# Kernel optimization log

Hardware: AMD Instinct MI355X
Metric: run time of the kernel (lower is better)

Reference implementation:

```python
import jax, jax.numpy as jnp
import numpy as np

B, CIN, NF, COUT, H, W = 128, 64, 16, 256, 20, 20


def _warp(features, f):
    # features: (B, Cin, r, c), f: (r, c, 2) flow offsets
    r, c = features.shape[2], features.shape[3]
    grid = jnp.stack(
        jnp.meshgrid(jnp.arange(r, dtype=f.dtype), jnp.arange(c, dtype=f.dtype), indexing='ij'),
        axis=-1,
    )  # (r, c, 2) base index map
    idx = grid + f  # index_map += inverse, inverse == flow[i] after double negation
    base = jnp.floor(idx)
    frac = jax.lax.stop_gradient(idx - base)  # torch detaches s and t
    s, t = frac[..., 0], frac[..., 1]
    b = base.astype(jnp.int32)
    bx, by = b[..., 0], b[..., 1]
    padded = jnp.pad(features, ((0, 0), (0, 0), (1, 1), (1, 1)))  # zero pad by 1

    def gather(ix, iy):
        cx = jnp.clip(ix, 0, r)
        cy = jnp.clip(iy, 0, c)
        return padded[:, :, cx + 1, cy + 1]  # (B, Cin, r, c)

    # NOTE: weight for base_10 is s*(1-t) in the original source (apparent bug,
    # should be (1-s)*t) -- replicated here for faithfulness.
    w00 = (1 - s) * (1 - t)
    w01 = s * (1 - t)
    w10 = s * (1 - t)
    w11 = s * t
    return (gather(bx, by) * w00 + gather(bx + 1, by) * w01
            + gather(bx, by + 1) * w10 + gather(bx + 1, by + 1) * w11)


def setup_inputs() -> dict:
    key = jax.random.key(0)
    k1, k2, k3, k4 = jax.random.split(key, 4)
    x = jax.random.normal(k1, (B, CIN, H, W), dtype=jnp.float32)
    flow = jax.random.normal(k2, (NF, H, W, 2), dtype=jnp.float32)
    combinator = jax.random.normal(k3, (COUT, CIN * NF), dtype=jnp.float32) / np.sqrt(CIN * NF)
    bias = jax.random.normal(k4, (COUT,), dtype=jnp.float32) / np.sqrt(CIN * NF)
    return {"x": x, "flow": flow, "combinator": combinator, "bias": bias}


def reference(x, flow, combinator, bias):
    # per-flow bilinear warp, vectorized over the flow axis
    warped = jax.vmap(lambda f: _warp(x, f))(flow)  # (nf, B, Cin, h, w)
    nf, b, cin, h, w = warped.shape
    # permute(1,3,4,2,0).reshape -> columns ordered channel-major, flow-minor
    feat = warped.transpose(1, 3, 4, 2, 0).reshape(b, h, w, cin * nf)
    out = jnp.einsum('bhwk,ok->bhwo', feat, combinator) + bias
    return out.transpose(0, 3, 1, 2)  # (B, Cout, h, w)
```

## Files before the change

### kernel.cpp

```cpp
#include <hip/hip_runtime.h>
#include <hip/hip_fp16.h>
#include <stdint.h>

#define BATCH 128
#define CIN   64
#define NFLOW 16
#define COUT  256
#define HH    20
#define WW    20
#define NPIX  400
#define KTOT  1024
#define PT    100
#define NPT   4
#define NTH   256
#define NFR   7
#define FLR   112

typedef __attribute__((ext_vector_type(8))) short sh8;
typedef __attribute__((ext_vector_type(4))) float f4;

__global__ void prep_w(const float* __restrict__ wg, __half* __restrict__ Wf) {
    int gid = blockIdx.x * 256 + threadIdx.x;
    int j8  = gid & 127;
    int row = gid >> 7;
    int kc16 = j8 >> 2;
    int h    = j8 & 3;
    __half* dst = Wf + ((size_t)(kc16 * 16 + (row >> 4)) * 64 + h * 16 + (row & 15)) * 8;
    #pragma unroll
    for (int j = 0; j < 8; ++j) {
        int kp = j8 * 8 + j;
        int kc = kp >> 6;
        int l  = kp & 63;
        int f  = (kc >> 3) * 8 + (l >> 3);
        int c  = (kc & 7) * 8 + (l & 7);
        dst[j] = __float2half(wg[(size_t)row * KTOT + c * NFLOW + f]);
    }
}

__global__ __launch_bounds__(NTH, 2) void flow_main(
    const float* __restrict__ xg, const __half* __restrict__ Wf,
    const float* __restrict__ flowg, const float* __restrict__ biasg,
    float* __restrict__ outg)
{
    __shared__ __align__(16) __half xb[CIN * NPIX];
    __shared__ __align__(16) __half fl[2][FLR * 64];

    const int bid0 = blockIdx.x;
    const int bid  = (bid0 & 7) * 64 + (bid0 >> 3);
    const int b  = bid >> 2;
    const int pt = bid & 3;
    const int p0 = pt * PT;

    const int tid  = threadIdx.x;
    const int wv   = tid >> 6;
    const int lane = tid & 63;
    const int lr   = lane & 15;
    const int hq   = lane >> 4;

    const float* xsrc = xg + (size_t)b * (CIN * NPIX);

    #pragma unroll
    for (int it = 0; it < 13; ++it) {
        int idx = it * NTH + tid;
        if (idx < 3200) {
            int cb  = idx / NPIX;
            int pix = idx - cb * NPIX;
            const float* s = xsrc + (size_t)(cb * 8) * NPIX + pix;
            __half2 h0 = __floats2half2_rn(s[0 * NPIX], s[1 * NPIX]);
            __half2 h1 = __floats2half2_rn(s[2 * NPIX], s[3 * NPIX]);
            __half2 h2 = __floats2half2_rn(s[4 * NPIX], s[5 * NPIX]);
            __half2 h3 = __floats2half2_rn(s[6 * NPIX], s[7 * NPIX]);
            uint4 pk;
            pk.x = __builtin_bit_cast(uint32_t, h0);
            pk.y = __builtin_bit_cast(uint32_t, h1);
            pk.z = __builtin_bit_cast(uint32_t, h2);
            pk.w = __builtin_bit_cast(uint32_t, h3);
            *(uint4*)&xb[(size_t)idx * 8] = pk;
        }
    }

    __half2 w2_[4][4];
    int     pb_[4][4];
    int     fo_[4];

    auto build_tables = [&](int fb) {
        #pragma unroll
        for (int g = 0; g < 4; ++g) {
            int it = g & 1;
            if (it == 0 || lane < PT - 64) {
                int fi = wv * 2 + (g >> 1);
                int p  = it * 64 + lane;
                int f  = fb * 8 + fi;
                int gp = p0 + p;
                int i = gp / WW;
                int j = gp - i * WW;
                float fx = flowg[((f * HH + i) * WW + j) * 2 + 0];
                float fy = flowg[((f * HH + i) * WW + j) * 2 + 1];
                float ax = (float)i + fx;
                float ay = (float)j + fy;
                float bxf = floorf(ax), byf = floorf(ay);
                float s = ax - bxf, t = ay - byf;
                int ibx = (int)bxf, iby = (int)byf;
                float w00 = (1.f - s) * (1.f - t);
                float w01 = s * (1.f - t);
                float w10 = s * (1.f - t);
                float w11 = s * t;
                int cx0 = min(max(ibx, 0), HH);
                int cx1 = min(max(ibx + 1, 0), HH);
                int cy0 = min(max(iby, 0), WW);
                int cy1 = min(max(iby + 1, 0), WW);
                int v0 = (cx0 < HH) & (cy0 < WW);
                int v1 = (cx1 < HH) & (cy0 < WW);
                int v2 = (cx0 < HH) & (cy1 < WW);
                int v3 = (cx1 < HH) & (cy1 < WW);
                w2_[g][0] = __half2half2(__float2half(v0 ? w00 : 0.f));
                w2_[g][1] = __half2half2(__float2half(v1 ? w01 : 0.f));
                w2_[g][2] = __half2half2(__float2half(v2 ? w10 : 0.f));
                w2_[g][3] = __half2half2(__float2half(v3 ? w11 : 0.f));
                pb_[g][0] = (v0 ? (cx0 * WW + cy0) : 0) * 16;
                pb_[g][1] = (v1 ? (cx1 * WW + cy0) : 0) * 16;
                pb_[g][2] = (v2 ? (cx0 * WW + cy1) : 0) * 16;
                pb_[g][3] = (v3 ? (cx1 * WW + cy1) : 0) * 16;
                fo_[g] = p * 128 + (((fi) ^ (p & 7)) << 4);
            }
        }
    };

    auto fill = [&](int k) {
        const char* xcb = (const char*)xb + (k & 7) * 6400;
        char* flb = (char*)fl[k & 1];
        #pragma unroll
        for (int g = 0; g < 4; ++g) {
            int it = g & 1;
            if (it == 0 || lane < PT - 64) {
                __half2 s0 = __builtin_bit_cast(__half2, 0u);
                __half2 s1 = s0, s2 = s0, s3 = s0;
                #pragma unroll
                for (int q = 0; q < 4; ++q) {
                    const uint4 d = *(const uint4*)(xcb + pb_[g][q]);
                    __half2 wq = w2_[g][q];
                    s0 = __hfma2(wq, __builtin_bit_cast(__half2, d.x), s0);
                    s1 = __hfma2(wq, __builtin_bit_cast(__half2, d.y), s1);
                    s2 = __hfma2(wq, __builtin_bit_cast(__half2, d.z), s2);
                    s3 = __hfma2(wq, __builtin_bit_cast(__half2, d.w), s3);
                }
                uint4 pk;
                pk.x = __builtin_bit_cast(uint32_t, s0);
                pk.y = __builtin_bit_cast(uint32_t, s1);
                pk.z = __builtin_bit_cast(uint32_t, s2);
                pk.w = __builtin_bit_cast(uint32_t, s3);
                *(uint4*)(flb + fo_[g]) = pk;
            }
        }
    };

    build_tables(0);
    __syncthreads();
    fill(0);
    __syncthreads();

    f4 acc[4][NFR] = {};

    const int q0 = (hq ^ (lr & 7)) << 4;

    for (int kc = 0; kc < 16; ++kc) {
        if (kc == 7) build_tables(1);

        const sh8* wfp = (const sh8*)Wf + (size_t)(2 * kc * 16 + 4 * wv) * 64 + lane;
        sh8 a0_0 = wfp[0],    a0_1 = wfp[64],   a0_2 = wfp[128],  a0_3 = wfp[192];
        sh8 a1_0 = wfp[1024], a1_1 = wfp[1088], a1_2 = wfp[1152], a1_3 = wfp[1216];

        if (kc <= 14) fill(kc + 1);

        const char* flr_b = (const char*)fl[kc & 1];
        __builtin_amdgcn_s_setprio(1);
        #pragma unroll
        for (int nf = 0; nf < NFR; ++nf) {
            int rowb = (nf * 16 + lr) * 128;
            sh8 b0 = *(const sh8*)(flr_b + (rowb + q0));
            sh8 b1 = *(const sh8*)(flr_b + ((rowb + q0) ^ 64));
            acc[0][nf] = __builtin_amdgcn_mfma_f32_16x16x32_f16(a0_0, b0, acc[0][nf], 0, 0, 0);
            acc[1][nf] = __builtin_amdgcn_mfma_f32_16x16x32_f16(a0_1, b0, acc[1][nf], 0, 0, 0);
            acc[2][nf] = __builtin_amdgcn_mfma_f32_16x16x32_f16(a0_2, b0, acc[2][nf], 0, 0, 0);
            acc[3][nf] = __builtin_amdgcn_mfma_f32_16x16x32_f16(a0_3, b0, acc[3][nf], 0, 0, 0);
            acc[0][nf] = __builtin_amdgcn_mfma_f32_16x16x32_f16(a1_0, b1, acc[0][nf], 0, 0, 0);
            acc[1][nf] = __builtin_amdgcn_mfma_f32_16x16x32_f16(a1_1, b1, acc[1][nf], 0, 0, 0);
            acc[2][nf] = __builtin_amdgcn_mfma_f32_16x16x32_f16(a1_2, b1, acc[2][nf], 0, 0, 0);
            acc[3][nf] = __builtin_amdgcn_mfma_f32_16x16x32_f16(a1_3, b1, acc[3][nf], 0, 0, 0);
        }
        __builtin_amdgcn_s_setprio(0);

        __syncthreads();
    }

    float* ob = outg + (size_t)b * (COUT * NPIX) + p0;
    #pragma unroll
    for (int mi = 0; mi < 4; ++mi) {
        #pragma unroll
        for (int r = 0; r < 4; ++r) {
            int m = wv * 64 + mi * 16 + hq * 4 + r;
            float bs = biasg[m];
            #pragma unroll
            for (int nf = 0; nf < NFR; ++nf) {
                if (nf < 6 || lr < 4)
                    ob[(size_t)m * NPIX + nf * 16 + lr] = acc[mi][nf][r] + bs;
            }
        }
    }
}

extern "C" void kernel_launch(void* const* d_in, const int* in_sizes, int n_in,
                              void* d_out, int out_size, void* d_ws, size_t ws_size,
                              hipStream_t stream) {
    const float* x    = (const float*)d_in[0];
    const float* flow = (const float*)d_in[1];
    const float* comb = (const float*)d_in[2];
    const float* bias = (const float*)d_in[3];
    float* out = (float*)d_out;

    __half* Wf = (__half*)d_ws;

    prep_w<<<dim3(128), dim3(256), 0, stream>>>(comb, Wf);
    flow_main<<<dim3(BATCH * NPT), dim3(NTH), 0, stream>>>(x, Wf, flow, bias, out);
}
```

Measured before the change: 50.74 us.

## Split waves into producer/consumer roles and process two pixel tiles per block

Doubles the block to 512 threads, with four waves building the bilinear-warped tiles in LDS and four waves running the MFMA GEMM on the other buffer. Each block now handles two pixel tiles of one batch, so the x-to-half conversion into shared memory is amortized across twice the work and the grid is halved. The intent is to overlap the gather/fill work with matrix-core work. The cost is fewer blocks for the GPU, a per-chunk barrier between roles, and register pressure under the unchanged launch bounds.

```diff
diff --git a/kernel.cpp b/kernel.cpp
--- a/kernel.cpp
+++ b/kernel.cpp
@@ -11,8 +11,7 @@
 #define NPIX  400
 #define KTOT  1024
 #define PT    100
-#define NPT   4
-#define NTH   256
+#define NTH   512
 #define NFR   7
 #define FLR   112
 
@@ -46,13 +45,14 @@
     __shared__ __align__(16) __half fl[2][FLR * 64];
 
     const int bid0 = blockIdx.x;
-    const int bid  = (bid0 & 7) * 64 + (bid0 >> 3);
-    const int b  = bid >> 2;
-    const int pt = bid & 3;
-    const int p0 = pt * PT;
+    const int bid  = (bid0 & 7) * 32 + (bid0 >> 3);
+    const int b  = bid >> 1;
+    const int tp = bid & 1;
 
     const int tid  = threadIdx.x;
     const int wv   = tid >> 6;
+    const bool prod = wv < 4;
+    const int cwv  = wv & 3;
     const int lane = tid & 63;
     const int lr   = lane & 15;
     const int hq   = lane >> 4;
@@ -60,7 +60,7 @@
     const float* xsrc = xg + (size_t)b * (CIN * NPIX);
 
     #pragma unroll
-    for (int it = 0; it < 13; ++it) {
+    for (int it = 0; it < 7; ++it) {
         int idx = it * NTH + tid;
         if (idx < 3200) {
             int cb  = idx / NPIX;
@@ -83,12 +83,12 @@
     int     pb_[4][4];
     int     fo_[4];
 
-    auto build_tables = [&](int fb) {
+    auto build_tables = [&](int fb, int p0) {
         #pragma unroll
         for (int g = 0; g < 4; ++g) {
             int it = g & 1;
             if (it == 0 || lane < PT - 64) {
-                int fi = wv * 2 + (g >> 1);
+                int fi = cwv * 2 + (g >> 1);
                 int p  = it * 64 + lane;
                 int f  = fb * 8 + fi;
                 int gp = p0 + p;
@@ -121,7 +121,7 @@
                 pb_[g][1] = (v1 ? (cx1 * WW + cy0) : 0) * 16;
                 pb_[g][2] = (v2 ? (cx0 * WW + cy1) : 0) * 16;
                 pb_[g][3] = (v3 ? (cx1 * WW + cy1) : 0) * 16;
-                fo_[g] = p * 128 + (((fi) ^ (p & 7)) << 4);
+                fo_[g] = p * 128 + ((fi ^ (p & 7)) << 4);
             }
         }
     };
@@ -154,56 +154,71 @@
         }
     };
 
-    build_tables(0);
     __syncthreads();
-    fill(0);
-    __syncthreads();
-
-    f4 acc[4][NFR] = {};
 
     const int q0 = (hq ^ (lr & 7)) << 4;
 
-    for (int kc = 0; kc < 16; ++kc) {
-        if (kc == 7) build_tables(1);
-
-        const sh8* wfp = (const sh8*)Wf + (size_t)(2 * kc * 16 + 4 * wv) * 64 + lane;
-        sh8 a0_0 = wfp[0],    a0_1 = wfp[64],   a0_2 = wfp[128],  a0_3 = wfp[192];
-        sh8 a1_0 = wfp[1024], a1_1 = wfp[1088], a1_2 = wfp[1152], a1_3 = wfp[1216];
-
-        if (kc <= 14) fill(kc + 1);
-
-        const char* flr_b = (const char*)fl[kc & 1];
-        __builtin_amdgcn_s_setprio(1);
-        #pragma unroll
-        for (int nf = 0; nf < NFR; ++nf) {
-            int rowb = (nf * 16 + lr) * 128;
-            sh8 b0 = *(const sh8*)(flr_b + (rowb + q0));
-            sh8 b1 = *(const sh8*)(flr_b + ((rowb + q0) ^ 64));
-            acc[0][nf] = __builtin_amdgcn_mfma_f32_16x16x32_f16(a0_0, b0, acc[0][nf], 0, 0, 0);
-            acc[1][nf] = __builtin_amdgcn_mfma_f32_16x16x32_f16(a0_1, b0, acc[1][nf], 0, 0, 0);
-            acc[2][nf] = __builtin_amdgcn_mfma_f32_16x16x32_f16(a0_2, b0, acc[2][nf], 0, 0, 0);
-            acc[3][nf] = __builtin_amdgcn_mfma_f32_16x16x32_f16(a0_3, b0, acc[3][nf], 0, 0, 0);
-            acc[0][nf] = __builtin_amdgcn_mfma_f32_16x16x32_f16(a1_0, b1, acc[0][nf], 0, 0, 0);
-            acc[1][nf] = __builtin_amdgcn_mfma_f32_16x16x32_f16(a1_1, b1, acc[1][nf], 0, 0, 0);
-            acc[2][nf] = __builtin_amdgcn_mfma_f32_16x16x32_f16(a1_2, b1, acc[2][nf], 0, 0, 0);
-            acc[3][nf] = __builtin_amdgcn_mfma_f32_16x16x32_f16(a1_3, b1, acc[3][nf], 0, 0, 0);
-        }
-        __builtin_amdgcn_s_setprio(0);
-
+    for (int t = 0; t < 2; ++t) {
+        const int p0 = tp * 200 + t * 100;
+
+        if (prod) { build_tables(0, p0); fill(0); }
         __syncthreads();
-    }
-
-    float* ob = outg + (size_t)b * (COUT * NPIX) + p0;
-    #pragma unroll
-    for (int mi = 0; mi < 4; ++mi) {
-        #pragma unroll
-        for (int r = 0; r < 4; ++r) {
-            int m = wv * 64 + mi * 16 + hq * 4 + r;
-            float bs = biasg[m];
+
+        f4 acc[4][NFR] = {};
+        sh8 a[8];
+
+        if (!prod) {
+            const sh8* wfp = (const sh8*)Wf + (size_t)(4 * cwv) * 64 + lane;
             #pragma unroll
-            for (int nf = 0; nf < NFR; ++nf) {
-                if (nf < 6 || lr < 4)
-                    ob[(size_t)m * NPIX + nf * 16 + lr] = acc[mi][nf][r] + bs;
+            for (int i = 0; i < 4; ++i) { a[i] = wfp[i * 64]; a[4 + i] = wfp[1024 + i * 64]; }
+        }
+
+        for (int kc = 0; kc < 16; ++kc) {
+            if (prod) {
+                if (kc == 7) build_tables(1, p0);
+                if (kc < 15) fill(kc + 1);
+            } else {
+                const char* flr_b = (const char*)fl[kc & 1];
+                __builtin_amdgcn_s_setprio(1);
+                #pragma unroll
+                for (int nf = 0; nf < NFR; ++nf) {
+                    int rowb = (nf * 16 + lr) * 128;
+                    sh8 b0 = *(const sh8*)(flr_b + (rowb + q0));
+                    sh8 b1 = *(const sh8*)(flr_b + ((rowb + q0) ^ 64));
+                    acc[0][nf] = __builtin_amdgcn_mfma_f32_16x16x32_f16(a[0], b0, acc[0][nf], 0, 0, 0);
+                    acc[1][nf] = __builtin_amdgcn_mfma_f32_16x16x32_f16(a[1], b0, acc[1][nf], 0, 0, 0);
+                    acc[2][nf] = __builtin_amdgcn_mfma_f32_16x16x32_f16(a[2], b0, acc[2][nf], 0, 0, 0);
+                    acc[3][nf] = __builtin_amdgcn_mfma_f32_16x16x32_f16(a[3], b0, acc[3][nf], 0, 0, 0);
+                    acc[0][nf] = __builtin_amdgcn_mfma_f32_16x16x32_f16(a[4], b1, acc[0][nf], 0, 0, 0);
+                    acc[1][nf] = __builtin_amdgcn_mfma_f32_16x16x32_f16(a[5], b1, acc[1][nf], 0, 0, 0);
+                    acc[2][nf] = __builtin_amdgcn_mfma_f32_16x16x32_f16(a[6], b1, acc[2][nf], 0, 0, 0);
+                    acc[3][nf] = __builtin_amdgcn_mfma_f32_16x16x32_f16(a[7], b1, acc[3][nf], 0, 0, 0);
+                }
+                __builtin_amdgcn_s_setprio(0);
+                if (kc < 15) {
+                    const sh8* wfp = (const sh8*)Wf
+                        + (size_t)(2 * (kc + 1) * 16 + 4 * cwv) * 64 + lane;
+                    #pragma unroll
+                    for (int i = 0; i < 4; ++i) { a[i] = wfp[i * 64]; a[4 + i] = wfp[1024 + i * 64]; }
+                }
+            }
+            __syncthreads();
+        }
+
+        if (!prod) {
+            float* ob = outg + (size_t)b * (COUT * NPIX) + p0;
+            #pragma unroll
+            for (int mi = 0; mi < 4; ++mi) {
+                #pragma unroll
+                for (int r = 0; r < 4; ++r) {
+                    int m = cwv * 64 + mi * 16 + hq * 4 + r;
+                    float bs = biasg[m];
+                    #pragma unroll
+                    for (int nf = 0; nf < NFR; ++nf) {
+                        if (nf < 6 || lr < 4)
+                            ob[(size_t)m * NPIX + nf * 16 + lr] = acc[mi][nf][r] + bs;
+                    }
+                }
             }
         }
     }
@@ -221,5 +236,5 @@
     __half* Wf = (__half*)d_ws;
 
     prep_w<<<dim3(128), dim3(256), 0, stream>>>(comb, Wf);
-    flow_main<<<dim3(BATCH * NPT), dim3(NTH), 0, stream>>>(x, Wf, flow, bias, out);
+    flow_main<<<dim3(BATCH * 2), dim3(NTH), 0, stream>>>(x, Wf, flow, bias, out);
 }
```

Result: slower. 60.45 us (+19.1%).
